# Performance work log

Measured on AMD Instinct MI355X. Metric: run time of the kernel, lower is better.

## Reference

```python
import jax, jax.numpy as jnp
import numpy as np
from jax import lax

H = 50  # hidden_size


def _lstm_layer(x, w_ih, w_hh, b_ih, b_hh):
    """Single LSTM layer, batch_first input x: [B, T, I]. PyTorch gate order i,f,g,o."""
    B = x.shape[0]
    # Precompute input projections for all timesteps: [B, T, 4H]
    x_proj = jnp.einsum('bti,gi->btg', x, w_ih) + b_ih + b_hh
    xs = jnp.swapaxes(x_proj, 0, 1)  # time-major [T, B, 4H]

    def step(carry, xp):
        h, c = carry
        gates = xp + h @ w_hh.T  # [B, 4H]
        i, f, g, o = jnp.split(gates, 4, axis=-1)
        i = jax.nn.sigmoid(i)
        f = jax.nn.sigmoid(f)
        g = jnp.tanh(g)
        o = jax.nn.sigmoid(o)
        c = f * c + i * g
        h = o * jnp.tanh(c)
        return (h, c), h

    h0 = jnp.zeros((B, H), dtype=x.dtype)
    c0 = jnp.zeros((B, H), dtype=x.dtype)
    (_, _), hs = lax.scan(step, (h0, c0), xs)
    return jnp.swapaxes(hs, 0, 1)  # back to [B, T, H]


def setup_inputs() -> dict:
    key = jax.random.key(0)
    ks = jax.random.split(key, 11)
    B, T = 512, 256
    I, O = 144, 144
    s = 0.1
    return {
        'x': jax.random.normal(ks[0], (B, T, 16, 9), dtype=jnp.float32),
        'w_ih0': jax.random.normal(ks[1], (4 * H, I), dtype=jnp.float32) * s,
        'w_hh0': jax.random.normal(ks[2], (4 * H, H), dtype=jnp.float32) * s,
        'b_ih0': jax.random.normal(ks[3], (4 * H,), dtype=jnp.float32) * s,
        'b_hh0': jax.random.normal(ks[4], (4 * H,), dtype=jnp.float32) * s,
        'w_ih1': jax.random.normal(ks[5], (4 * H, H), dtype=jnp.float32) * s,
        'w_hh1': jax.random.normal(ks[6], (4 * H, H), dtype=jnp.float32) * s,
        'b_ih1': jax.random.normal(ks[7], (4 * H,), dtype=jnp.float32) * s,
        'b_hh1': jax.random.normal(ks[8], (4 * H,), dtype=jnp.float32) * s,
        'w_fc': jax.random.normal(ks[9], (O, H), dtype=jnp.float32) * s,
        'b_fc': jax.random.normal(ks[10], (O,), dtype=jnp.float32) * s,
    }


def reference(x, w_ih0, w_hh0, b_ih0, b_hh0, w_ih1, w_hh1, b_ih1, b_hh1, w_fc, b_fc):
    B, T = x.shape[0], x.shape[1]
    x = x.reshape(B, T, -1)  # [B, T, 144]
    h1 = _lstm_layer(x, w_ih0, w_hh0, b_ih0, b_hh0)   # [B, T, H]
    h2 = _lstm_layer(h1, w_ih1, w_hh1, b_ih1, b_hh1)  # [B, T, H] (dropout inactive in eval)
    last = h2[:, -1, :]                               # [B, H]
    out = last @ w_fc.T + b_fc                        # [B, 144]
    return out.reshape(-1, 16, 9)
```

## Files before the change

### kernel.cpp

```cpp
#include <hip/hip_runtime.h>
#include <hip/hip_fp16.h>
#include <cstdint>
#include <cstddef>

#define H    50
#define TT   256
#define BATCH 512
#define KDIM 144
#define ODIM 144
#define NW   32
#define WS   8

typedef _Float16 half8  __attribute__((ext_vector_type(8)));
typedef _Float16 half4v __attribute__((ext_vector_type(4)));
typedef float    floatx4 __attribute__((ext_vector_type(4)));
typedef int      int4v  __attribute__((ext_vector_type(4)));

__device__ __forceinline__ float rcpf(float x) { return __builtin_amdgcn_rcpf(x); }
__device__ __forceinline__ float sigm(float x) { return rcpf(1.0f + __expf(-x)); }
__device__ __forceinline__ float tanhx(float x) {
    return 1.0f - 2.0f * rcpf(__expf(2.0f * x) + 1.0f);
}

__device__ __forceinline__ void sync_lds() {
    asm volatile("s_waitcnt lgkmcnt(0)\n\ts_barrier" ::: "memory");
}
__device__ __forceinline__ void wave_lds_fence() {
    asm volatile("s_waitcnt lgkmcnt(0)" ::: "memory");
}

__device__ __forceinline__ half8 make_hh(const float* __restrict__ Wt,
                                         int kkA, int gate, int q, int s) {
    const float* r0 = Wt + (size_t)(gate * H + (kkA < H ? kkA : 0)) * H;
    half8 r;
    #pragma unroll
    for (int j = 0; j < 8; ++j) {
        const int k = s * 32 + q * 8 + j;
        r[j] = (_Float16)((kkA < H && k < H) ? r0[k] : 0.0f);
    }
    return r;
}
__device__ __forceinline__ half8 make_ax(const float* __restrict__ Wih0,
                                         const float* __restrict__ bih0,
                                         const float* __restrict__ bhh0,
                                         int kkA, int gate, int q, int s) {
    const int p = gate * H + (kkA < H ? kkA : 0);
    half8 r;
    #pragma unroll
    for (int j = 0; j < 8; ++j) {
        const int k = s * 32 + q * 8 + j;
        float v = 0.0f;
        if (kkA < H) {
            if (k < KDIM)        v = Wih0[(size_t)p * KDIM + k];
            else if (k == KDIM)  v = bih0[p] + bhh0[p];
        }
        r[j] = (_Float16)v;
    }
    return r;
}
__device__ __forceinline__ half8 make_p1(const float* __restrict__ Wih1,
                                         const float* __restrict__ bih1,
                                         const float* __restrict__ bhh1,
                                         int kkA, int gate, int q, int s) {
    const int p = gate * H + (kkA < H ? kkA : 0);
    half8 r;
    #pragma unroll
    for (int j = 0; j < 8; ++j) {
        const int k = s * 32 + q * 8 + j;
        float v = 0.0f;
        if (kkA < H) {
            if (k < H)           v = Wih1[(size_t)p * H + k];
            else if (k == H)     v = bih1[p] + bhh1[p];
        }
        r[j] = (_Float16)v;
    }
    return r;
}

__global__ __launch_bounds__(512, 1) void lstm_fused(
    const float* __restrict__ X,
    const float* __restrict__ Whh0, const float* __restrict__ Wih0,
    const float* __restrict__ bih0, const float* __restrict__ bhh0,
    const float* __restrict__ Wih1, const float* __restrict__ Whh1,
    const float* __restrict__ bih1, const float* __restrict__ bhh1,
    const float* __restrict__ Wfc, const float* __restrict__ bfc,
    float* __restrict__ out)
{
    const int b0   = blockIdx.x * 2;
    const int tid  = threadIdx.x;
    const int lane = tid & 63;
    const int w    = tid >> 6;
    const int col  = lane & 15;
    const int q    = lane >> 4;

    __shared__ __align__(16) _Float16 B0[2][2][4][16][8];
    __shared__ __align__(16) _Float16 B1[2][2][4][16][8];
    __shared__ __align__(16) _Float16 HW[2][2][4][16][8];
    __shared__ __align__(16) float    gp0[64 * 72];
    __shared__ __align__(16) float    gp1[64 * 72];
    __shared__ __align__(16) float    scr[8][2][2][8][4];
    __shared__ __align__(16) _Float16 XB[2][5][4][16][8];
    __shared__ float h1f[2][52];

    int4v Ap[22];
    {
        const int prow = lane & 15;
        const int gate = prow & 3;
        const int kkA0 = 8 * w + 0 + (prow >> 2);
        const int kkA1 = 8 * w + 4 + (prow >> 2);
        Ap[0] = __builtin_bit_cast(int4v, make_hh(Whh0, kkA0, gate, q, 0));
        Ap[1] = __builtin_bit_cast(int4v, make_hh(Whh0, kkA0, gate, q, 1));
        Ap[2] = __builtin_bit_cast(int4v, make_hh(Whh0, kkA1, gate, q, 0));
        Ap[3] = __builtin_bit_cast(int4v, make_hh(Whh0, kkA1, gate, q, 1));
        #pragma unroll
        for (int s = 0; s < 5; ++s) Ap[4 + s] = __builtin_bit_cast(int4v, make_ax(Wih0, bih0, bhh0, kkA0, gate, q, s));
        #pragma unroll
        for (int s = 0; s < 5; ++s) Ap[9 + s] = __builtin_bit_cast(int4v, make_ax(Wih0, bih0, bhh0, kkA1, gate, q, s));
        Ap[14] = __builtin_bit_cast(int4v, make_hh(Whh1, kkA0, gate, q, 0));
        Ap[15] = __builtin_bit_cast(int4v, make_hh(Whh1, kkA0, gate, q, 1));
        Ap[16] = __builtin_bit_cast(int4v, make_hh(Whh1, kkA1, gate, q, 0));
        Ap[17] = __builtin_bit_cast(int4v, make_hh(Whh1, kkA1, gate, q, 1));
        Ap[18] = __builtin_bit_cast(int4v, make_p1(Wih1, bih1, bhh1, kkA0, gate, q, 0));
        Ap[19] = __builtin_bit_cast(int4v, make_p1(Wih1, bih1, bhh1, kkA0, gate, q, 1));
        Ap[20] = __builtin_bit_cast(int4v, make_p1(Wih1, bih1, bhh1, kkA1, gate, q, 0));
        Ap[21] = __builtin_bit_cast(int4v, make_p1(Wih1, bih1, bhh1, kkA1, gate, q, 1));
    }
    #pragma unroll
    for (int i = 0; i < 22; ++i) asm volatile("" : "+a"(Ap[i]));

    const bool act  = lane < 32;
    const int  aL   = (lane >> 4) & 1;
    const int  atl  = (lane >> 3) & 1;
    const int  aidx = lane & 7;
    const int  au   = 8 * w + 4 * atl + (aidx >> 1);
    const int  acol = aidx & 1;
    float c = 0.0f;

    const int cs1 = tid / 36,         kk1 = tid % 36;
    const int cs2 = (tid + 512) / 36, kk2 = (tid + 512) % 36;
    const float* xp1 = X + ((size_t)(b0 + (cs1 & 1)) * TT + (cs1 >> 1)) * KDIM + kk1 * 4;
    const float* xp2 = X + ((size_t)(b0 + (cs2 & 1)) * TT + (cs2 >> 1)) * KDIM + kk2 * 4;

    for (int i = tid; i < 1024; i += 512) { ((int*)B0)[i] = 0; ((int*)B1)[i] = 0; ((int*)HW)[i] = 0; }
    for (int i = tid; i < 2560; i += 512) ((int*)XB)[i] = 0;
    __syncthreads();
    if (tid < 32) {
        HW[tid >> 4][1][2][tid & 15][2] = (_Float16)1.0f;
        XB[tid >> 4][4][2][tid & 15][0] = (_Float16)1.0f;
    }
    {
        const float4 v1 = *(const float4*)xp1;
        const int s = kk1 >> 3, qq = (kk1 >> 1) & 3, j0 = (kk1 & 1) * 4;
        half4v h; h[0]=(_Float16)v1.x; h[1]=(_Float16)v1.y; h[2]=(_Float16)v1.z; h[3]=(_Float16)v1.w;
        *(half4v*)&XB[0][s][qq][cs1][j0] = h;
        if (tid < 64) {
            const float4 v2 = *(const float4*)xp2;
            const int s2 = kk2 >> 3, q2 = (kk2 >> 1) & 3, j2 = (kk2 & 1) * 4;
            half4v h2; h2[0]=(_Float16)v2.x; h2[1]=(_Float16)v2.y; h2[2]=(_Float16)v2.z; h2[3]=(_Float16)v2.w;
            *(half4v*)&XB[0][s2][q2][cs2][j2] = h2;
        }
    }
    __syncthreads();

    const int gb = (col >> 1) * 8 + (col & 1) * 4;

    for (int W = 0; W < NW; ++W) {
        #pragma unroll
        for (int i = 0; i < 22; ++i) asm volatile("" : "+a"(Ap[i]));
        const int cb = W & 1, nb = cb ^ 1, pb = cb ^ 1;
        const bool more = (W + 1) < NW;
        float4 xv1 = make_float4(0.f,0.f,0.f,0.f), xv2 = make_float4(0.f,0.f,0.f,0.f);
        if (more) {
            xv1 = *(const float4*)(xp1 + (size_t)(W + 1) * WS * KDIM);
            if (tid < 64) xv2 = *(const float4*)(xp2 + (size_t)(W + 1) * WS * KDIM);
        }
        {
            half8 xbf[5];
            #pragma unroll
            for (int s = 0; s < 5; ++s) xbf[s] = *(const half8*)&XB[cb][s][q][col][0];
            floatx4 px0 = (floatx4)(0.0f), px1 = (floatx4)(0.0f);
            #pragma unroll
            for (int s = 0; s < 5; ++s) {
                px0 = __builtin_amdgcn_mfma_f32_16x16x32_f16(__builtin_bit_cast(half8, Ap[4 + s]), xbf[s], px0, 0, 0, 0);
                px1 = __builtin_amdgcn_mfma_f32_16x16x32_f16(__builtin_bit_cast(half8, Ap[9 + s]), xbf[s], px1, 0, 0, 0);
            }
            *(floatx4*)&gp0[(8 * w + q) * 72 + gb]     = px0;
            *(floatx4*)&gp0[(8 * w + 4 + q) * 72 + gb] = px1;
        }
        if (W > 0) {
            half8 hbf[2];
            #pragma unroll
            for (int s = 0; s < 2; ++s) hbf[s] = *(const half8*)&HW[pb][s][q][col][0];
            floatx4 pw0 = (floatx4)(0.0f), pw1 = (floatx4)(0.0f);
            #pragma unroll
            for (int s = 0; s < 2; ++s) {
                pw0 = __builtin_amdgcn_mfma_f32_16x16x32_f16(__builtin_bit_cast(half8, Ap[18 + s]), hbf[s], pw0, 0, 0, 0);
                pw1 = __builtin_amdgcn_mfma_f32_16x16x32_f16(__builtin_bit_cast(half8, Ap[20 + s]), hbf[s], pw1, 0, 0, 0);
            }
            *(floatx4*)&gp1[(8 * w + q) * 72 + gb]     = pw0;
            *(floatx4*)&gp1[(8 * w + 4 + q) * 72 + gb] = pw1;
        }
        #pragma unroll
        for (int i = 0; i < WS; ++i) {
            const int rb = i & 1, wb = rb ^ 1;
            half8 bf0[2], bf1[2];
            #pragma unroll
            for (int s = 0; s < 2; ++s) {
                bf0[s] = *(const half8*)&B0[rb][s][q][col][0];
                bf1[s] = *(const half8*)&B1[rb][s][q][col][0];
            }
            floatx4 a0[2], a1[2];
            #pragma unroll
            for (int tl = 0; tl < 2; ++tl) { a0[tl] = (floatx4)(0.0f); a1[tl] = (floatx4)(0.0f); }
            __builtin_amdgcn_s_setprio(1);
            #pragma unroll
            for (int tl = 0; tl < 2; ++tl) {
                #pragma unroll
                for (int s = 0; s < 2; ++s) {
                    a0[tl] = __builtin_amdgcn_mfma_f32_16x16x32_f16(__builtin_bit_cast(half8, Ap[tl*2+s]),    bf0[s], a0[tl], 0, 0, 0);
                    a1[tl] = __builtin_amdgcn_mfma_f32_16x16x32_f16(__builtin_bit_cast(half8, Ap[14+tl*2+s]), bf1[s], a1[tl], 0, 0, 0);
                }
            }
            __builtin_amdgcn_s_setprio(0);
            if (col < 2) {
                #pragma unroll
                for (int tl = 0; tl < 2; ++tl) {
                    *(floatx4*)&scr[w][0][tl][q * 2 + col][0] = a0[tl];
                    *(floatx4*)&scr[w][1][tl][q * 2 + col][0] = a1[tl];
                }
            }
            wave_lds_fence();
            if (act && (aL == 0 || W > 0)) {
                const float* gpb = aL ? gp1 : gp0;
                floatx4 g = *(const floatx4*)&scr[w][aL][atl][aidx][0];
                const floatx4 gx = *(const floatx4*)&gpb[au * 72 + i * 8 + acol * 4];
                g[0] += gx[0]; g[1] += gx[1]; g[2] += gx[2]; g[3] += gx[3];
                const float gi = sigm(g[0]), gf = sigm(g[1]);
                const float gg = tanhx(g[2]), go = sigm(g[3]);
                c = gf * c + gi * gg;
                const float hv = go * tanhx(c);
                if (au < H) {
                    const _Float16 h16 = (_Float16)hv;
                    if (aL == 0) {
                        B0[wb][au >> 5][(au >> 3) & 3][acol][au & 7] = h16;
                        HW[cb][au >> 5][(au >> 3) & 3][2 * i + acol][au & 7] = h16;
                    } else {
                        B1[wb][au >> 5][(au >> 3) & 3][acol][au & 7] = h16;
                    }
                }
            }
            if (i == 3 && more) {
                {
                    const int s = kk1 >> 3, qq = (kk1 >> 1) & 3, j0 = (kk1 & 1) * 4;
                    half4v h; h[0]=(_Float16)xv1.x; h[1]=(_Float16)xv1.y; h[2]=(_Float16)xv1.z; h[3]=(_Float16)xv1.w;
                    *(half4v*)&XB[nb][s][qq][cs1][j0] = h;
                }
                if (tid < 64) {
                    const int s2 = kk2 >> 3, q2 = (kk2 >> 1) & 3, j2 = (kk2 & 1) * 4;
                    half4v h2; h2[0]=(_Float16)xv2.x; h2[1]=(_Float16)xv2.y; h2[2]=(_Float16)xv2.z; h2[3]=(_Float16)xv2.w;
                    *(half4v*)&XB[nb][s2][q2][cs2][j2] = h2;
                }
            }
            sync_lds();
        }
    }
    {
        #pragma unroll
        for (int i = 0; i < 22; ++i) asm volatile("" : "+a"(Ap[i]));
        {
            half8 hbf[2];
            #pragma unroll
            for (int s = 0; s < 2; ++s) hbf[s] = *(const half8*)&HW[(NW - 1) & 1][s][q][col][0];
            floatx4 pw0 = (floatx4)(0.0f), pw1 = (floatx4)(0.0f);
            #pragma unroll
            for (int s = 0; s < 2; ++s) {
                pw0 = __builtin_amdgcn_mfma_f32_16x16x32_f16(__builtin_bit_cast(half8, Ap[18 + s]), hbf[s], pw0, 0, 0, 0);
                pw1 = __builtin_amdgcn_mfma_f32_16x16x32_f16(__builtin_bit_cast(half8, Ap[20 + s]), hbf[s], pw1, 0, 0, 0);
            }
            *(floatx4*)&gp1[(8 * w + q) * 72 + gb]     = pw0;
            *(floatx4*)&gp1[(8 * w + 4 + q) * 72 + gb] = pw1;
        }
        #pragma unroll
        for (int i = 0; i < WS; ++i) {
            const int rb = i & 1, wb = rb ^ 1;
            half8 bf1[2];
            #pragma unroll
            for (int s = 0; s < 2; ++s) bf1[s] = *(const half8*)&B1[rb][s][q][col][0];
            floatx4 a1[2];
            #pragma unroll
            for (int tl = 0; tl < 2; ++tl) {
                a1[tl] = (floatx4)(0.0f);
                #pragma unroll
                for (int s = 0; s < 2; ++s)
                    a1[tl] = __builtin_amdgcn_mfma_f32_16x16x32_f16(__builtin_bit_cast(half8, Ap[14+tl*2+s]), bf1[s], a1[tl], 0, 0, 0);
            }
            if (col < 2) {
                #pragma unroll
                for (int tl = 0; tl < 2; ++tl)
                    *(floatx4*)&scr[w][1][tl][q * 2 + col][0] = a1[tl];
            }
            wave_lds_fence();
            if (act && aL == 1) {
                floatx4 g = *(const floatx4*)&scr[w][1][atl][aidx][0];
                const floatx4 gx = *(const floatx4*)&gp1[au * 72 + i * 8 + acol * 4];
                g[0] += gx[0]; g[1] += gx[1]; g[2] += gx[2]; g[3] += gx[3];
                const float gi = sigm(g[0]), gf = sigm(g[1]);
                const float gg = tanhx(g[2]), go = sigm(g[3]);
                c = gf * c + gi * gg;
                const float hv = go * tanhx(c);
                if (au < H) {
                    B1[wb][au >> 5][(au >> 3) & 3][acol][au & 7] = (_Float16)hv;
                    if (i == WS - 1) h1f[acol][au] = hv;
                }
            }
            sync_lds();
        }
    }
    if (tid < 2 * ODIM) {
        const int r = tid / ODIM, o = tid - r * ODIM;
        float s = bfc[o];
        const float* wr = Wfc + (size_t)o * H;
        #pragma unroll
        for (int k = 0; k < H; ++k) s += wr[k] * h1f[r][k];
        out[(size_t)(b0 + r) * ODIM + o] = s;
    }
}

extern "C" void kernel_launch(void* const* d_in, const int* in_sizes, int n_in,
                              void* d_out, int out_size, void* d_ws, size_t ws_size,
                              hipStream_t stream) {
    const float* x    = (const float*)d_in[0];
    const float* wih0 = (const float*)d_in[1];
    const float* whh0 = (const float*)d_in[2];
    const float* bih0 = (const float*)d_in[3];
    const float* bhh0 = (const float*)d_in[4];
    const float* wih1 = (const float*)d_in[5];
    const float* whh1 = (const float*)d_in[6];
    const float* bih1 = (const float*)d_in[7];
    const float* bhh1 = (const float*)d_in[8];
    const float* wfc  = (const float*)d_in[9];
    const float* bfc  = (const float*)d_in[10];
    float* outp = (float*)d_out;

    lstm_fused<<<BATCH / 2, 512, 0, stream>>>(x, whh0, wih0, bih0, bhh0,
                                              wih1, whh1, bih1, bhh1,
                                              wfc, bfc, outp);
}
```

Baseline: 297.4 us.

## Halve block to 4 waves, give each wave 16 hidden units, gather gates in registers

```diff
diff --git a/kernel.cpp b/kernel.cpp
--- a/kernel.cpp
+++ b/kernel.cpp
@@ -77,7 +77,7 @@
     return r;
 }
 
-__global__ __launch_bounds__(512, 1) void lstm_fused(
+__global__ __launch_bounds__(256, 1) void lstm_fused(
     const float* __restrict__ X,
     const float* __restrict__ Whh0, const float* __restrict__ Wih0,
     const float* __restrict__ bih0, const float* __restrict__ bhh0,
@@ -93,71 +93,69 @@
     const int col  = lane & 15;
     const int q    = lane >> 4;
 
-    __shared__ __align__(16) _Float16 B0[2][2][4][16][8];
-    __shared__ __align__(16) _Float16 B1[2][2][4][16][8];
+    __shared__ __align__(16) _Float16 B0[2][2][4][2][8];
+    __shared__ __align__(16) _Float16 B1[2][2][4][2][8];
     __shared__ __align__(16) _Float16 HW[2][2][4][16][8];
     __shared__ __align__(16) float    gp0[64 * 72];
     __shared__ __align__(16) float    gp1[64 * 72];
-    __shared__ __align__(16) float    scr[8][2][2][8][4];
     __shared__ __align__(16) _Float16 XB[2][5][4][16][8];
     __shared__ float h1f[2][52];
 
-    int4v Ap[22];
+    int4v Ap[44];
     {
         const int prow = lane & 15;
         const int gate = prow & 3;
-        const int kkA0 = 8 * w + 0 + (prow >> 2);
-        const int kkA1 = 8 * w + 4 + (prow >> 2);
-        Ap[0] = __builtin_bit_cast(int4v, make_hh(Whh0, kkA0, gate, q, 0));
-        Ap[1] = __builtin_bit_cast(int4v, make_hh(Whh0, kkA0, gate, q, 1));
-        Ap[2] = __builtin_bit_cast(int4v, make_hh(Whh0, kkA1, gate, q, 0));
-        Ap[3] = __builtin_bit_cast(int4v, make_hh(Whh0, kkA1, gate, q, 1));
-        #pragma unroll
-        for (int s = 0; s < 5; ++s) Ap[4 + s] = __builtin_bit_cast(int4v, make_ax(Wih0, bih0, bhh0, kkA0, gate, q, s));
-        #pragma unroll
-        for (int s = 0; s < 5; ++s) Ap[9 + s] = __builtin_bit_cast(int4v, make_ax(Wih0, bih0, bhh0, kkA1, gate, q, s));
-        Ap[14] = __builtin_bit_cast(int4v, make_hh(Whh1, kkA0, gate, q, 0));
-        Ap[15] = __builtin_bit_cast(int4v, make_hh(Whh1, kkA0, gate, q, 1));
-        Ap[16] = __builtin_bit_cast(int4v, make_hh(Whh1, kkA1, gate, q, 0));
-        Ap[17] = __builtin_bit_cast(int4v, make_hh(Whh1, kkA1, gate, q, 1));
-        Ap[18] = __builtin_bit_cast(int4v, make_p1(Wih1, bih1, bhh1, kkA0, gate, q, 0));
-        Ap[19] = __builtin_bit_cast(int4v, make_p1(Wih1, bih1, bhh1, kkA0, gate, q, 1));
-        Ap[20] = __builtin_bit_cast(int4v, make_p1(Wih1, bih1, bhh1, kkA1, gate, q, 0));
-        Ap[21] = __builtin_bit_cast(int4v, make_p1(Wih1, bih1, bhh1, kkA1, gate, q, 1));
+        #pragma unroll
+        for (int tl = 0; tl < 4; ++tl) {
+            const int kkA = 16 * w + 4 * tl + (prow >> 2);
+            #pragma unroll
+            for (int s = 0; s < 2; ++s) Ap[tl * 2 + s]      = __builtin_bit_cast(int4v, make_hh(Whh0, kkA, gate, q, s));
+            #pragma unroll
+            for (int s = 0; s < 5; ++s) Ap[8 + tl * 5 + s]  = __builtin_bit_cast(int4v, make_ax(Wih0, bih0, bhh0, kkA, gate, q, s));
+            #pragma unroll
+            for (int s = 0; s < 2; ++s) Ap[28 + tl * 2 + s] = __builtin_bit_cast(int4v, make_hh(Whh1, kkA, gate, q, s));
+            #pragma unroll
+            for (int s = 0; s < 2; ++s) Ap[36 + tl * 2 + s] = __builtin_bit_cast(int4v, make_p1(Wih1, bih1, bhh1, kkA, gate, q, s));
+        }
     }
     #pragma unroll
-    for (int i = 0; i < 22; ++i) asm volatile("" : "+a"(Ap[i]));
-
-    const bool act  = lane < 32;
-    const int  aL   = (lane >> 4) & 1;
-    const int  atl  = (lane >> 3) & 1;
-    const int  aidx = lane & 7;
-    const int  au   = 8 * w + 4 * atl + (aidx >> 1);
-    const int  acol = aidx & 1;
+    for (int i = 0; i < 44; ++i) asm volatile("" : "+a"(Ap[i]));
+
+    const int  c2  = col >> 1;
+    const int  r   = col & 1;
+    const int  atl = c2 & 3;
+    const int  aL  = c2 >> 2;
+    const int  au  = 16 * w + 4 * atl + q;
+    const bool areal = (au < H);
     float c = 0.0f;
-
-    const int cs1 = tid / 36,         kk1 = tid % 36;
-    const int cs2 = (tid + 512) / 36, kk2 = (tid + 512) % 36;
-    const float* xp1 = X + ((size_t)(b0 + (cs1 & 1)) * TT + (cs1 >> 1)) * KDIM + kk1 * 4;
-    const float* xp2 = X + ((size_t)(b0 + (cs2 & 1)) * TT + (cs2 >> 1)) * KDIM + kk2 * 4;
-
-    for (int i = tid; i < 1024; i += 512) { ((int*)B0)[i] = 0; ((int*)B1)[i] = 0; ((int*)HW)[i] = 0; }
-    for (int i = tid; i < 2560; i += 512) ((int*)XB)[i] = 0;
+    const float* gpb = (aL ? gp1 : gp0) + au * 72;
+
+    const int cs1 = tid / 36,          kk1 = tid % 36;
+    const int cs2 = (tid + 256) / 36,  kk2 = (tid + 256) % 36;
+    const int cs3 = (tid + 512) / 36,  kk3 = (tid + 512) % 36;
+    const float* xq1 = X + ((size_t)(b0 + (cs1 & 1)) * TT + (cs1 >> 1)) * KDIM + kk1 * 4;
+    const float* xq2 = X + ((size_t)(b0 + (cs2 & 1)) * TT + (cs2 >> 1)) * KDIM + kk2 * 4;
+    const float* xq3 = X + ((size_t)(b0 + (cs3 & 1)) * TT + (cs3 >> 1)) * KDIM + kk3 * 4;
+
+    if (tid < 128) { ((int*)B0)[tid] = 0; ((int*)B1)[tid] = 0; }
+    for (int i = tid; i < 1024; i += 256) ((int*)HW)[i] = 0;
+    for (int i = tid; i < 2560; i += 256) ((int*)XB)[i] = 0;
     __syncthreads();
     if (tid < 32) {
         HW[tid >> 4][1][2][tid & 15][2] = (_Float16)1.0f;
         XB[tid >> 4][4][2][tid & 15][0] = (_Float16)1.0f;
     }
     {
-        const float4 v1 = *(const float4*)xp1;
-        const int s = kk1 >> 3, qq = (kk1 >> 1) & 3, j0 = (kk1 & 1) * 4;
+        const float4 v1 = *(const float4*)xq1;
         half4v h; h[0]=(_Float16)v1.x; h[1]=(_Float16)v1.y; h[2]=(_Float16)v1.z; h[3]=(_Float16)v1.w;
-        *(half4v*)&XB[0][s][qq][cs1][j0] = h;
+        *(half4v*)&XB[0][kk1 >> 3][(kk1 >> 1) & 3][cs1][(kk1 & 1) * 4] = h;
+        const float4 v2 = *(const float4*)xq2;
+        half4v h2; h2[0]=(_Float16)v2.x; h2[1]=(_Float16)v2.y; h2[2]=(_Float16)v2.z; h2[3]=(_Float16)v2.w;
+        *(half4v*)&XB[0][kk2 >> 3][(kk2 >> 1) & 3][cs2][(kk2 & 1) * 4] = h2;
         if (tid < 64) {
-            const float4 v2 = *(const float4*)xp2;
-            const int s2 = kk2 >> 3, q2 = (kk2 >> 1) & 3, j2 = (kk2 & 1) * 4;
-            half4v h2; h2[0]=(_Float16)v2.x; h2[1]=(_Float16)v2.y; h2[2]=(_Float16)v2.z; h2[3]=(_Float16)v2.w;
-            *(half4v*)&XB[0][s2][q2][cs2][j2] = h2;
+            const float4 v3 = *(const float4*)xq3;
+            half4v h3; h3[0]=(_Float16)v3.x; h3[1]=(_Float16)v3.y; h3[2]=(_Float16)v3.z; h3[3]=(_Float16)v3.w;
+            *(half4v*)&XB[0][kk3 >> 3][(kk3 >> 1) & 3][cs3][(kk3 & 1) * 4] = h3;
         }
     }
     __syncthreads();
@@ -166,99 +164,98 @@
 
     for (int W = 0; W < NW; ++W) {
         #pragma unroll
-        for (int i = 0; i < 22; ++i) asm volatile("" : "+a"(Ap[i]));
+        for (int i = 0; i < 44; ++i) asm volatile("" : "+a"(Ap[i]));
         const int cb = W & 1, nb = cb ^ 1, pb = cb ^ 1;
         const bool more = (W + 1) < NW;
-        float4 xv1 = make_float4(0.f,0.f,0.f,0.f), xv2 = make_float4(0.f,0.f,0.f,0.f);
+        float4 xv1, xv2, xv3;
         if (more) {
-            xv1 = *(const float4*)(xp1 + (size_t)(W + 1) * WS * KDIM);
-            if (tid < 64) xv2 = *(const float4*)(xp2 + (size_t)(W + 1) * WS * KDIM);
+            xv1 = *(const float4*)(xq1 + (size_t)(W + 1) * WS * KDIM);
+            xv2 = *(const float4*)(xq2 + (size_t)(W + 1) * WS * KDIM);
+            if (tid < 64) xv3 = *(const float4*)(xq3 + (size_t)(W + 1) * WS * KDIM);
         }
         {
             half8 xbf[5];
             #pragma unroll
             for (int s = 0; s < 5; ++s) xbf[s] = *(const half8*)&XB[cb][s][q][col][0];
-            floatx4 px0 = (floatx4)(0.0f), px1 = (floatx4)(0.0f);
-            #pragma unroll
-            for (int s = 0; s < 5; ++s) {
-                px0 = __builtin_amdgcn_mfma_f32_16x16x32_f16(__builtin_bit_cast(half8, Ap[4 + s]), xbf[s], px0, 0, 0, 0);
-                px1 = __builtin_amdgcn_mfma_f32_16x16x32_f16(__builtin_bit_cast(half8, Ap[9 + s]), xbf[s], px1, 0, 0, 0);
-            }
-            *(floatx4*)&gp0[(8 * w + q) * 72 + gb]     = px0;
-            *(floatx4*)&gp0[(8 * w + 4 + q) * 72 + gb] = px1;
+            #pragma unroll
+            for (int tl = 0; tl < 4; ++tl) {
+                floatx4 px = (floatx4)(0.0f);
+                #pragma unroll
+                for (int s = 0; s < 5; ++s)
+                    px = __builtin_amdgcn_mfma_f32_16x16x32_f16(__builtin_bit_cast(half8, Ap[8 + tl * 5 + s]), xbf[s], px, 0, 0, 0);
+                *(floatx4*)&gp0[(16 * w + 4 * tl + q) * 72 + gb] = px;
+            }
         }
         if (W > 0) {
             half8 hbf[2];
             #pragma unroll
             for (int s = 0; s < 2; ++s) hbf[s] = *(const half8*)&HW[pb][s][q][col][0];
-            floatx4 pw0 = (floatx4)(0.0f), pw1 = (floatx4)(0.0f);
-            #pragma unroll
-            for (int s = 0; s < 2; ++s) {
-                pw0 = __builtin_amdgcn_mfma_f32_16x16x32_f16(__builtin_bit_cast(half8, Ap[18 + s]), hbf[s], pw0, 0, 0, 0);
-                pw1 = __builtin_amdgcn_mfma_f32_16x16x32_f16(__builtin_bit_cast(half8, Ap[20 + s]), hbf[s], pw1, 0, 0, 0);
-            }
-            *(floatx4*)&gp1[(8 * w + q) * 72 + gb]     = pw0;
-            *(floatx4*)&gp1[(8 * w + 4 + q) * 72 + gb] = pw1;
-        }
+            #pragma unroll
+            for (int tl = 0; tl < 4; ++tl) {
+                floatx4 pw = (floatx4)(0.0f);
+                #pragma unroll
+                for (int s = 0; s < 2; ++s)
+                    pw = __builtin_amdgcn_mfma_f32_16x16x32_f16(__builtin_bit_cast(half8, Ap[36 + tl * 2 + s]), hbf[s], pw, 0, 0, 0);
+                *(floatx4*)&gp1[(16 * w + 4 * tl + q) * 72 + gb] = pw;
+            }
+        }
+        wave_lds_fence();
         #pragma unroll
         for (int i = 0; i < WS; ++i) {
             const int rb = i & 1, wb = rb ^ 1;
             half8 bf0[2], bf1[2];
             #pragma unroll
             for (int s = 0; s < 2; ++s) {
-                bf0[s] = *(const half8*)&B0[rb][s][q][col][0];
-                bf1[s] = *(const half8*)&B1[rb][s][q][col][0];
-            }
-            floatx4 a0[2], a1[2];
-            #pragma unroll
-            for (int tl = 0; tl < 2; ++tl) { a0[tl] = (floatx4)(0.0f); a1[tl] = (floatx4)(0.0f); }
-            __builtin_amdgcn_s_setprio(1);
-            #pragma unroll
-            for (int tl = 0; tl < 2; ++tl) {
+                bf0[s] = *(const half8*)&B0[rb][s][q][r][0];
+                bf1[s] = *(const half8*)&B1[rb][s][q][r][0];
+            }
+            const floatx4 gx = *(const floatx4*)&gpb[i * 8 + r * 4];
+            floatx4 a0[4], a1[4];
+            #pragma unroll
+            for (int tl = 0; tl < 4; ++tl) { a0[tl] = (floatx4)(0.0f); a1[tl] = (floatx4)(0.0f); }
+            #pragma unroll
+            for (int tl = 0; tl < 4; ++tl) {
                 #pragma unroll
                 for (int s = 0; s < 2; ++s) {
                     a0[tl] = __builtin_amdgcn_mfma_f32_16x16x32_f16(__builtin_bit_cast(half8, Ap[tl*2+s]),    bf0[s], a0[tl], 0, 0, 0);
-                    a1[tl] = __builtin_amdgcn_mfma_f32_16x16x32_f16(__builtin_bit_cast(half8, Ap[14+tl*2+s]), bf1[s], a1[tl], 0, 0, 0);
-                }
-            }
-            __builtin_amdgcn_s_setprio(0);
-            if (col < 2) {
-                #pragma unroll
-                for (int tl = 0; tl < 2; ++tl) {
-                    *(floatx4*)&scr[w][0][tl][q * 2 + col][0] = a0[tl];
-                    *(floatx4*)&scr[w][1][tl][q * 2 + col][0] = a1[tl];
-                }
-            }
-            wave_lds_fence();
-            if (act && (aL == 0 || W > 0)) {
-                const float* gpb = aL ? gp1 : gp0;
-                floatx4 g = *(const floatx4*)&scr[w][aL][atl][aidx][0];
-                const floatx4 gx = *(const floatx4*)&gpb[au * 72 + i * 8 + acol * 4];
+                    a1[tl] = __builtin_amdgcn_mfma_f32_16x16x32_f16(__builtin_bit_cast(half8, Ap[28+tl*2+s]), bf1[s], a1[tl], 0, 0, 0);
+                }
+            }
+            floatx4 g;
+            #pragma unroll
+            for (int gi_ = 0; gi_ < 4; ++gi_) {
+                const float s01 = (c2 & 1) ? a0[1][gi_] : a0[0][gi_];
+                const float s23 = (c2 & 1) ? a0[3][gi_] : a0[2][gi_];
+                const float s45 = (c2 & 1) ? a1[1][gi_] : a1[0][gi_];
+                const float s67 = (c2 & 1) ? a1[3][gi_] : a1[2][gi_];
+                const float e0  = (c2 & 2) ? s23 : s01;
+                const float e1  = (c2 & 2) ? s67 : s45;
+                g[gi_] = (c2 & 4) ? e1 : e0;
+            }
+            if (aL == 0 || W > 0) {
                 g[0] += gx[0]; g[1] += gx[1]; g[2] += gx[2]; g[3] += gx[3];
                 const float gi = sigm(g[0]), gf = sigm(g[1]);
                 const float gg = tanhx(g[2]), go = sigm(g[3]);
                 c = gf * c + gi * gg;
                 const float hv = go * tanhx(c);
-                if (au < H) {
+                if (areal) {
                     const _Float16 h16 = (_Float16)hv;
                     if (aL == 0) {
-                        B0[wb][au >> 5][(au >> 3) & 3][acol][au & 7] = h16;
-                        HW[cb][au >> 5][(au >> 3) & 3][2 * i + acol][au & 7] = h16;
+                        B0[wb][au >> 5][(au >> 3) & 3][r][au & 7] = h16;
+                        HW[cb][au >> 5][(au >> 3) & 3][2 * i + r][au & 7] = h16;
                     } else {
-                        B1[wb][au >> 5][(au >> 3) & 3][acol][au & 7] = h16;
+                        B1[wb][au >> 5][(au >> 3) & 3][r][au & 7] = h16;
                     }
                 }
             }
             if (i == 3 && more) {
-                {
-                    const int s = kk1 >> 3, qq = (kk1 >> 1) & 3, j0 = (kk1 & 1) * 4;
-                    half4v h; h[0]=(_Float16)xv1.x; h[1]=(_Float16)xv1.y; h[2]=(_Float16)xv1.z; h[3]=(_Float16)xv1.w;
-                    *(half4v*)&XB[nb][s][qq][cs1][j0] = h;
-                }
+                half4v h; h[0]=(_Float16)xv1.x; h[1]=(_Float16)xv1.y; h[2]=(_Float16)xv1.z; h[3]=(_Float16)xv1.w;
+                *(half4v*)&XB[nb][kk1 >> 3][(kk1 >> 1) & 3][cs1][(kk1 & 1) * 4] = h;
+                half4v h2; h2[0]=(_Float16)xv2.x; h2[1]=(_Float16)xv2.y; h2[2]=(_Float16)xv2.z; h2[3]=(_Float16)xv2.w;
+                *(half4v*)&XB[nb][kk2 >> 3][(kk2 >> 1) & 3][cs2][(kk2 & 1) * 4] = h2;
                 if (tid < 64) {
-                    const int s2 = kk2 >> 3, q2 = (kk2 >> 1) & 3, j2 = (kk2 & 1) * 4;
-                    half4v h2; h2[0]=(_Float16)xv2.x; h2[1]=(_Float16)xv2.y; h2[2]=(_Float16)xv2.z; h2[3]=(_Float16)xv2.w;
-                    *(half4v*)&XB[nb][s2][q2][cs2][j2] = h2;
+                    half4v h3; h3[0]=(_Float16)xv3.x; h3[1]=(_Float16)xv3.y; h3[2]=(_Float16)xv3.z; h3[3]=(_Float16)xv3.w;
+                    *(half4v*)&XB[nb][kk3 >> 3][(kk3 >> 1) & 3][cs3][(kk3 & 1) * 4] = h3;
                 }
             }
             sync_lds();
@@ -266,63 +263,64 @@
     }
     {
         #pragma unroll
-        for (int i = 0; i < 22; ++i) asm volatile("" : "+a"(Ap[i]));
+        for (int i = 0; i < 44; ++i) asm volatile("" : "+a"(Ap[i]));
         {
             half8 hbf[2];
             #pragma unroll
             for (int s = 0; s < 2; ++s) hbf[s] = *(const half8*)&HW[(NW - 1) & 1][s][q][col][0];
-            floatx4 pw0 = (floatx4)(0.0f), pw1 = (floatx4)(0.0f);
-            #pragma unroll
-            for (int s = 0; s < 2; ++s) {
-                pw0 = __builtin_amdgcn_mfma_f32_16x16x32_f16(__builtin_bit_cast(half8, Ap[18 + s]), hbf[s], pw0, 0, 0, 0);
-                pw1 = __builtin_amdgcn_mfma_f32_16x16x32_f16(__builtin_bit_cast(half8, Ap[20 + s]), hbf[s], pw1, 0, 0, 0);
-            }
-            *(floatx4*)&gp1[(8 * w + q) * 72 + gb]     = pw0;
-            *(floatx4*)&gp1[(8 * w + 4 + q) * 72 + gb] = pw1;
-        }
+            #pragma unroll
+            for (int tl = 0; tl < 4; ++tl) {
+                floatx4 pw = (floatx4)(0.0f);
+                #pragma unroll
+                for (int s = 0; s < 2; ++s)
+                    pw = __builtin_amdgcn_mfma_f32_16x16x32_f16(__builtin_bit_cast(half8, Ap[36 + tl * 2 + s]), hbf[s], pw, 0, 0, 0);
+                *(floatx4*)&gp1[(16 * w + 4 * tl + q) * 72 + gb] = pw;
+            }
+        }
+        wave_lds_fence();
         #pragma unroll
         for (int i = 0; i < WS; ++i) {
             const int rb = i & 1, wb = rb ^ 1;
             half8 bf1[2];
             #pragma unroll
-            for (int s = 0; s < 2; ++s) bf1[s] = *(const half8*)&B1[rb][s][q][col][0];
-            floatx4 a1[2];
-            #pragma unroll
-            for (int tl = 0; tl < 2; ++tl) {
+            for (int s = 0; s < 2; ++s) bf1[s] = *(const half8*)&B1[rb][s][q][r][0];
+            const floatx4 gx = *(const floatx4*)&gpb[i * 8 + r * 4];
+            floatx4 a1[4];
+            #pragma unroll
+            for (int tl = 0; tl < 4; ++tl) {
                 a1[tl] = (floatx4)(0.0f);
                 #pragma unroll
                 for (int s = 0; s < 2; ++s)
-                    a1[tl] = __builtin_amdgcn_mfma_f32_16x16x32_f16(__builtin_bit_cast(half8, Ap[14+tl*2+s]), bf1[s], a1[tl], 0, 0, 0);
-            }
-            if (col < 2) {
-                #pragma unroll
-                for (int tl = 0; tl < 2; ++tl)
-                    *(floatx4*)&scr[w][1][tl][q * 2 + col][0] = a1[tl];
-            }
-            wave_lds_fence();
-            if (act && aL == 1) {
-                floatx4 g = *(const floatx4*)&scr[w][1][atl][aidx][0];
-                const floatx4 gx = *(const floatx4*)&gp1[au * 72 + i * 8 + acol * 4];
+                    a1[tl] = __builtin_amdgcn_mfma_f32_16x16x32_f16(__builtin_bit_cast(half8, Ap[28+tl*2+s]), bf1[s], a1[tl], 0, 0, 0);
+            }
+            if (aL == 1) {
+                floatx4 g;
+                #pragma unroll
+                for (int gi_ = 0; gi_ < 4; ++gi_) {
+                    const float s01 = (c2 & 1) ? a1[1][gi_] : a1[0][gi_];
+                    const float s23 = (c2 & 1) ? a1[3][gi_] : a1[2][gi_];
+                    g[gi_] = (c2 & 2) ? s23 : s01;
+                }
                 g[0] += gx[0]; g[1] += gx[1]; g[2] += gx[2]; g[3] += gx[3];
                 const float gi = sigm(g[0]), gf = sigm(g[1]);
                 const float gg = tanhx(g[2]), go = sigm(g[3]);
                 c = gf * c + gi * gg;
                 const float hv = go * tanhx(c);
-                if (au < H) {
-                    B1[wb][au >> 5][(au >> 3) & 3][acol][au & 7] = (_Float16)hv;
-                    if (i == WS - 1) h1f[acol][au] = hv;
+                if (areal) {
+                    B1[wb][au >> 5][(au >> 3) & 3][r][au & 7] = (_Float16)hv;
+                    if (i == WS - 1) h1f[r][au] = hv;
                 }
             }
             sync_lds();
         }
     }
-    if (tid < 2 * ODIM) {
-        const int r = tid / ODIM, o = tid - r * ODIM;
+    for (int oo = tid; oo < 2 * ODIM; oo += 256) {
+        const int rr = oo / ODIM, o = oo - rr * ODIM;
         float s = bfc[o];
         const float* wr = Wfc + (size_t)o * H;
         #pragma unroll
-        for (int k = 0; k < H; ++k) s += wr[k] * h1f[r][k];
-        out[(size_t)(b0 + r) * ODIM + o] = s;
+        for (int k = 0; k < H; ++k) s += wr[k] * h1f[rr][k];
+        out[(size_t)(b0 + rr) * ODIM + o] = s;
     }
 }
 
@@ -342,7 +340,7 @@
     const float* bfc  = (const float*)d_in[10];
     float* outp = (float*)d_out;
 
-    lstm_fused<<<BATCH / 2, 512, 0, stream>>>(x, whh0, wih0, bih0, bhh0,
+    lstm_fused<<<BATCH / 2, 256, 0, stream>>>(x, whh0, wih0, bih0, bhh0,
                                               wih1, whh1, bih1, bhh1,
                                               wfc, bfc, outp);
 }
```

Result: slower. 309.0 us (+3.9%).

## Compute gate activations directly from MFMA registers, removing LDS scratch round-trip

Applied to the files above, without the earlier changes.

```diff
diff --git a/kernel.cpp b/kernel.cpp
--- a/kernel.cpp
+++ b/kernel.cpp
@@ -93,12 +93,11 @@
     const int col  = lane & 15;
     const int q    = lane >> 4;
 
-    __shared__ __align__(16) _Float16 B0[2][2][4][16][8];
-    __shared__ __align__(16) _Float16 B1[2][2][4][16][8];
+    __shared__ __align__(16) _Float16 B0[2][2][4][2][8];
+    __shared__ __align__(16) _Float16 B1[2][2][4][2][8];
     __shared__ __align__(16) _Float16 HW[2][2][4][16][8];
     __shared__ __align__(16) float    gp0[64 * 72];
     __shared__ __align__(16) float    gp1[64 * 72];
-    __shared__ __align__(16) float    scr[8][2][2][8][4];
     __shared__ __align__(16) _Float16 XB[2][5][4][16][8];
     __shared__ float h1f[2][52];
 
@@ -128,20 +127,23 @@
     #pragma unroll
     for (int i = 0; i < 22; ++i) asm volatile("" : "+a"(Ap[i]));
 
-    const bool act  = lane < 32;
-    const int  aL   = (lane >> 4) & 1;
-    const int  atl  = (lane >> 3) & 1;
-    const int  aidx = lane & 7;
-    const int  au   = 8 * w + 4 * atl + (aidx >> 1);
-    const int  acol = aidx & 1;
+    const int  c2m  = (col >> 1) & 3;
+    const int  r    = col & 1;
+    const int  atl  = c2m & 1;
+    const int  aL   = c2m >> 1;
+    const int  au   = 8 * w + 4 * atl + q;
+    const bool valid = (col < 8);
+    const bool areal = (au < H);
     float c = 0.0f;
+    const float* gpb = (aL ? gp1 : gp0) + au * 72;
 
     const int cs1 = tid / 36,         kk1 = tid % 36;
     const int cs2 = (tid + 512) / 36, kk2 = (tid + 512) % 36;
     const float* xp1 = X + ((size_t)(b0 + (cs1 & 1)) * TT + (cs1 >> 1)) * KDIM + kk1 * 4;
     const float* xp2 = X + ((size_t)(b0 + (cs2 & 1)) * TT + (cs2 >> 1)) * KDIM + kk2 * 4;
 
-    for (int i = tid; i < 1024; i += 512) { ((int*)B0)[i] = 0; ((int*)B1)[i] = 0; ((int*)HW)[i] = 0; }
+    if (tid < 128) { ((int*)B0)[tid] = 0; ((int*)B1)[tid] = 0; }
+    for (int i = tid; i < 1024; i += 512) ((int*)HW)[i] = 0;
     for (int i = tid; i < 2560; i += 512) ((int*)XB)[i] = 0;
     __syncthreads();
     if (tid < 32) {
@@ -169,7 +171,7 @@
         for (int i = 0; i < 22; ++i) asm volatile("" : "+a"(Ap[i]));
         const int cb = W & 1, nb = cb ^ 1, pb = cb ^ 1;
         const bool more = (W + 1) < NW;
-        float4 xv1 = make_float4(0.f,0.f,0.f,0.f), xv2 = make_float4(0.f,0.f,0.f,0.f);
+        float4 xv1, xv2;
         if (more) {
             xv1 = *(const float4*)(xp1 + (size_t)(W + 1) * WS * KDIM);
             if (tid < 64) xv2 = *(const float4*)(xp2 + (size_t)(W + 1) * WS * KDIM);
@@ -200,19 +202,20 @@
             *(floatx4*)&gp1[(8 * w + q) * 72 + gb]     = pw0;
             *(floatx4*)&gp1[(8 * w + 4 + q) * 72 + gb] = pw1;
         }
+        wave_lds_fence();
         #pragma unroll
         for (int i = 0; i < WS; ++i) {
             const int rb = i & 1, wb = rb ^ 1;
             half8 bf0[2], bf1[2];
             #pragma unroll
             for (int s = 0; s < 2; ++s) {
-                bf0[s] = *(const half8*)&B0[rb][s][q][col][0];
-                bf1[s] = *(const half8*)&B1[rb][s][q][col][0];
-            }
+                bf0[s] = *(const half8*)&B0[rb][s][q][r][0];
+                bf1[s] = *(const half8*)&B1[rb][s][q][r][0];
+            }
+            const floatx4 gx = *(const floatx4*)&gpb[i * 8 + r * 4];
             floatx4 a0[2], a1[2];
             #pragma unroll
             for (int tl = 0; tl < 2; ++tl) { a0[tl] = (floatx4)(0.0f); a1[tl] = (floatx4)(0.0f); }
-            __builtin_amdgcn_s_setprio(1);
             #pragma unroll
             for (int tl = 0; tl < 2; ++tl) {
                 #pragma unroll
@@ -221,32 +224,27 @@
                     a1[tl] = __builtin_amdgcn_mfma_f32_16x16x32_f16(__builtin_bit_cast(half8, Ap[14+tl*2+s]), bf1[s], a1[tl], 0, 0, 0);
                 }
             }
-            __builtin_amdgcn_s_setprio(0);
-            if (col < 2) {
-                #pragma unroll
-                for (int tl = 0; tl < 2; ++tl) {
-                    *(floatx4*)&scr[w][0][tl][q * 2 + col][0] = a0[tl];
-                    *(floatx4*)&scr[w][1][tl][q * 2 + col][0] = a1[tl];
-                }
-            }
-            wave_lds_fence();
-            if (act && (aL == 0 || W > 0)) {
-                const float* gpb = aL ? gp1 : gp0;
-                floatx4 g = *(const floatx4*)&scr[w][aL][atl][aidx][0];
-                const floatx4 gx = *(const floatx4*)&gpb[au * 72 + i * 8 + acol * 4];
-                g[0] += gx[0]; g[1] += gx[1]; g[2] += gx[2]; g[3] += gx[3];
-                const float gi = sigm(g[0]), gf = sigm(g[1]);
-                const float gg = tanhx(g[2]), go = sigm(g[3]);
-                c = gf * c + gi * gg;
-                const float hv = go * tanhx(c);
-                if (au < H) {
-                    const _Float16 h16 = (_Float16)hv;
-                    if (aL == 0) {
-                        B0[wb][au >> 5][(au >> 3) & 3][acol][au & 7] = h16;
-                        HW[cb][au >> 5][(au >> 3) & 3][2 * i + acol][au & 7] = h16;
-                    } else {
-                        B1[wb][au >> 5][(au >> 3) & 3][acol][au & 7] = h16;
-                    }
+            floatx4 g;
+            #pragma unroll
+            for (int gi_ = 0; gi_ < 4; ++gi_) {
+                const float s01 = (c2m & 1) ? a0[1][gi_] : a0[0][gi_];
+                const float s23 = (c2m & 1) ? a1[1][gi_] : a1[0][gi_];
+                g[gi_] = (c2m & 2) ? s23 : s01;
+            }
+            g[0] += gx[0]; g[1] += gx[1]; g[2] += gx[2]; g[3] += gx[3];
+            const float gi = sigm(g[0]), gf = sigm(g[1]);
+            const float gg = tanhx(g[2]), go = sigm(g[3]);
+            const bool en = (aL == 0) || (W > 0);
+            const float cn = gf * c + gi * gg;
+            c = en ? cn : c;
+            const float hv = go * tanhx(c);
+            if (valid && areal && en) {
+                const _Float16 h16 = (_Float16)hv;
+                if (aL == 0) {
+                    B0[wb][au >> 5][(au >> 3) & 3][r][au & 7] = h16;
+                    HW[cb][au >> 5][(au >> 3) & 3][2 * i + r][au & 7] = h16;
+                } else {
+                    B1[wb][au >> 5][(au >> 3) & 3][r][au & 7] = h16;
                 }
             }
             if (i == 3 && more) {
@@ -280,12 +278,14 @@
             *(floatx4*)&gp1[(8 * w + q) * 72 + gb]     = pw0;
             *(floatx4*)&gp1[(8 * w + 4 + q) * 72 + gb] = pw1;
         }
+        wave_lds_fence();
         #pragma unroll
         for (int i = 0; i < WS; ++i) {
             const int rb = i & 1, wb = rb ^ 1;
             half8 bf1[2];
             #pragma unroll
-            for (int s = 0; s < 2; ++s) bf1[s] = *(const half8*)&B1[rb][s][q][col][0];
+            for (int s = 0; s < 2; ++s) bf1[s] = *(const half8*)&B1[rb][s][q][r][0];
+            const floatx4 gx = *(const floatx4*)&gpb[i * 8 + r * 4];
             floatx4 a1[2];
             #pragma unroll
             for (int tl = 0; tl < 2; ++tl) {
@@ -294,35 +294,31 @@
                 for (int s = 0; s < 2; ++s)
                     a1[tl] = __builtin_amdgcn_mfma_f32_16x16x32_f16(__builtin_bit_cast(half8, Ap[14+tl*2+s]), bf1[s], a1[tl], 0, 0, 0);
             }
-            if (col < 2) {
-                #pragma unroll
-                for (int tl = 0; tl < 2; ++tl)
-                    *(floatx4*)&scr[w][1][tl][q * 2 + col][0] = a1[tl];
-            }
-            wave_lds_fence();
-            if (act && aL == 1) {
-                floatx4 g = *(const floatx4*)&scr[w][1][atl][aidx][0];
-                const floatx4 gx = *(const floatx4*)&gp1[au * 72 + i * 8 + acol * 4];
-                g[0] += gx[0]; g[1] += gx[1]; g[2] += gx[2]; g[3] += gx[3];
-                const float gi = sigm(g[0]), gf = sigm(g[1]);
-                const float gg = tanhx(g[2]), go = sigm(g[3]);
-                c = gf * c + gi * gg;
-                const float hv = go * tanhx(c);
-                if (au < H) {
-                    B1[wb][au >> 5][(au >> 3) & 3][acol][au & 7] = (_Float16)hv;
-                    if (i == WS - 1) h1f[acol][au] = hv;
-                }
+            floatx4 g;
+            #pragma unroll
+            for (int gi_ = 0; gi_ < 4; ++gi_)
+                g[gi_] = (c2m & 1) ? a1[1][gi_] : a1[0][gi_];
+            g[0] += gx[0]; g[1] += gx[1]; g[2] += gx[2]; g[3] += gx[3];
+            const float gi = sigm(g[0]), gf = sigm(g[1]);
+            const float gg = tanhx(g[2]), go = sigm(g[3]);
+            const bool en = (aL == 1);
+            const float cn = gf * c + gi * gg;
+            c = en ? cn : c;
+            const float hv = go * tanhx(c);
+            if (valid && en && areal) {
+                B1[wb][au >> 5][(au >> 3) & 3][r][au & 7] = (_Float16)hv;
+                if (i == WS - 1) h1f[r][au] = hv;
             }
             sync_lds();
         }
     }
     if (tid < 2 * ODIM) {
-        const int r = tid / ODIM, o = tid - r * ODIM;
+        const int rr = tid / ODIM, o = tid - rr * ODIM;
         float s = bfc[o];
         const float* wr = Wfc + (size_t)o * H;
         #pragma unroll
-        for (int k = 0; k < H; ++k) s += wr[k] * h1f[r][k];
-        out[(size_t)(b0 + r) * ODIM + o] = s;
+        for (int k = 0; k < H; ++k) s += wr[k] * h1f[rr][k];
+        out[(size_t)(b0 + rr) * ODIM + o] = s;
     }
 }
 
```

Measured after the change: 255.9 us. -14.0%, faster.
